# Optimization experiments

Measured on AMD Instinct MI355X. Metric: run time of the kernel, lower is better.

The kernel has to match this reference:

```python
import jax, jax.numpy as jnp
import numpy as np

IN_FEATURE = 4096
OUT_FEATURE = 4096
BLOCK_SIZE = 128
NUM_BLOCKS = IN_FEATURE // BLOCK_SIZE


def setup_inputs() -> dict:
    key = jax.random.key(0)
    k1, k2 = jax.random.split(key)
    x = jax.random.normal(k1, (4, 2048, IN_FEATURE), dtype=jnp.float32)
    # weight laid out as the original nn.Linear: [out_feature, in_feature]
    weight = jax.random.normal(k2, (OUT_FEATURE, IN_FEATURE), dtype=jnp.float32) * (1.0 / np.sqrt(IN_FEATURE))
    return {"x": x, "weight": weight}


def reference(x, weight):
    # The grouped 1x1 conv + reduce-sum over blocks is exactly a blockwise
    # matmul summed over blocks, i.e. out = x @ weight.T.
    # Expressed per-block to mirror the original structure without the
    # conv/permute/reshape overhead:
    b, s, in_f = x.shape
    xb = x.reshape(b, s, NUM_BLOCKS, BLOCK_SIZE)            # [b,s,nb,k]
    wb = weight.reshape(OUT_FEATURE, NUM_BLOCKS, BLOCK_SIZE)  # [o,nb,k]
    # sum over blocks (nb) and block_size (k) == full contraction over in_feature
    out = jnp.einsum('bsnk,onk->bso', xb, wb)
    return out
```

## Files before the change

### kernel.cpp

```cpp
#include <hip/hip_runtime.h>
#include <hip/hip_bf16.h>
#include <stdint.h>


typedef __bf16 bf16x8 __attribute__((ext_vector_type(8)));
typedef float f32x4 __attribute__((ext_vector_type(4)));

__device__ __forceinline__ unsigned short f2bf(float f) {
  unsigned u = __builtin_bit_cast(unsigned, f);
  u += 0x7FFFu + ((u >> 16) & 1u);
  return (unsigned short)(u >> 16);
}

__global__ void cvt_f32_to_bf16(const float* __restrict__ src,
                                unsigned short* __restrict__ dst, long n4) {
  long i = (long)blockIdx.x * blockDim.x + threadIdx.x;
  const long stride = (long)gridDim.x * blockDim.x;
  for (; i < n4; i += stride) {
    float4 v = reinterpret_cast<const float4*>(src)[i];
    ushort4 o;
    o.x = f2bf(v.x); o.y = f2bf(v.y); o.z = f2bf(v.z); o.w = f2bf(v.w);
    reinterpret_cast<ushort4*>(dst)[i] = o;
  }
}

__device__ __forceinline__ void gload_lds16(const void* g, void* lds) {
  __builtin_amdgcn_global_load_lds(
      (__attribute__((address_space(1))) void*)(g),
      (__attribute__((address_space(3))) void*)(lds), 16, 0, 0);
}

#define BARRIER()                                    \
  do {                                               \
    asm volatile("" ::: "memory");                   \
    __builtin_amdgcn_s_barrier();                    \
    asm volatile("" ::: "memory");                   \
  } while (0)
#define WAIT_LGKM0() asm volatile("s_waitcnt lgkmcnt(0)" ::: "memory")
#define WAIT_VM4() asm volatile("s_waitcnt vmcnt(4)" ::: "memory")
#define WAIT_VM0() asm volatile("s_waitcnt vmcnt(0)" ::: "memory")

#define READ_A(AB, LO)                                                      \
  _Pragma("unroll") for (int mi = 0; mi < 4; ++mi) {                        \
    const int row_ = ((LO)*4 + mi) * 16 + lr;                               \
    fa[(LO)*4 + mi][0] = *(const bf16x8*)((AB) + row_ * 128 + sx0);         \
    fa[(LO)*4 + mi][1] = *(const bf16x8*)((AB) + row_ * 128 + sx1);         \
  }
#define READ_B(BB, LO)                                                      \
  _Pragma("unroll") for (int ni = 0; ni < 2; ++ni) {                        \
    const int row_ = brow0 + ((LO)*2 + ni) * 16 + lr;                       \
    fb[(LO)*2 + ni][0] = *(const bf16x8*)((BB) + row_ * 128 + sx0);         \
    fb[(LO)*2 + ni][1] = *(const bf16x8*)((BB) + row_ * 128 + sx1);         \
  }
#define MQ(M0, N0)                                                          \
  _Pragma("unroll") for (int kk = 0; kk < 2; ++kk)                          \
  _Pragma("unroll") for (int mi = 0; mi < 4; ++mi)                          \
  _Pragma("unroll") for (int ni = 0; ni < 2; ++ni)                          \
      acc[(M0) + mi][(N0) + ni] = __builtin_amdgcn_mfma_f32_16x16x32_bf16(  \
          fa[(M0) + mi][kk], fb[(N0) + ni][kk], acc[(M0) + mi][(N0) + ni],  \
          0, 0, 0);

#define PH(READS, STAGES, M0, N0, WAITS)  \
  do {                                    \
    READS STAGES BARRIER();               \
    WAIT_LGKM0();                         \
    __builtin_amdgcn_s_setprio(1);        \
    MQ(M0, N0)                            \
    __builtin_amdgcn_s_setprio(0);        \
    WAITS BARRIER();                      \
  } while (0)

__global__ __launch_bounds__(512, 2) void gemm256(
    const unsigned short* __restrict__ A, const unsigned short* __restrict__ B,
    float* __restrict__ C, int M, int N, int K) {
  __shared__ __attribute__((aligned(1024))) char lds[131072];
  const int A00 = 0, A01 = 16384, A10 = 32768, A11 = 49152;
  const int B00 = 65536, B01 = 81920, B10 = 98304, B11 = 114688;

  const int t = threadIdx.x;
  const int l = t & 63;
  const int w = t >> 6;
  const int wm = w >> 2;
  const int wn = w & 3;
  const int q = l >> 4;
  const int lr = l & 15;
  const int xc = (lr & 7) << 4;
  const int sx0 = (q * 16) ^ xc;
  const int sx1 = (64 + q * 16) ^ xc;
  const int brow0 = (wn & 1) * 64;
  const int srow = l >> 3;
  const int sslot = ((l & 7) ^ ((l >> 3) & 7)) * 8;

  const int nwg = gridDim.x;
  int swz = blockIdx.x;
  if ((nwg & 7) == 0) swz = (swz & 7) * (nwg >> 3) + (swz >> 3);
  const int ntx = N >> 8;
  const int bx = swz % ntx;
  const int by = swz / ntx;
  const int mBase = by * 256, nBase = bx * 256;

  const char* Ard0 = lds + wm * 16384;
  const char* Ard1 = lds + 32768 + wm * 16384;
  const char* Brd0 = lds + 65536 + (wn >> 1) * 16384;
  const char* Brd1 = lds + 98304 + (wn >> 1) * 16384;

  bf16x8 fa[8][2], fb[4][2];
  f32x4 acc[8][4] = {};

  auto STAGE = [&](const unsigned short* __restrict__ G, int row0, int k0,
                   int ldsOff) {
    const unsigned short* s =
        G + (size_t)(row0 + w * 8 + srow) * K + k0 + sslot;
    char* d = lds + ldsOff + w * 1024;
    gload_lds16(s, d);
    gload_lds16(s + (size_t)64 * K, d + 8192);
  };

  STAGE(A, mBase, 0, A00);
  STAGE(A, mBase + 128, 0, A01);
  STAGE(B, nBase, 0, B00);
  STAGE(B, nBase + 128, 0, B01);
  STAGE(B, nBase, 64, B10);
  STAGE(A, mBase, 64, A10);
  WAIT_VM4();
  BARRIER();

  const int itermain = K / 128 - 1;
  for (int i = 0; i < itermain; ++i) {
    const int kA = (2 * i + 1) * 64;
    const int kB = kA + 64;
    const int kC = kB + 64;
    PH(READ_A(Ard0, 0) READ_B(Brd0, 0), STAGE(A, mBase + 128, kA, A11);, 0, 0, );
    PH(READ_B(Brd0, 1),                 STAGE(B, nBase + 128, kA, B11);, 0, 2, );
    PH(READ_A(Ard0, 1),                 STAGE(B, nBase,       kB, B00);, 4, 0, );
    PH(,                                STAGE(A, mBase,       kB, A00);, 4, 2, WAIT_VM4(););
    PH(READ_A(Ard1, 0) READ_B(Brd1, 0), STAGE(A, mBase + 128, kB, A01);, 0, 0, );
    PH(READ_B(Brd1, 1),                 STAGE(B, nBase + 128, kB, B01);, 0, 2, );
    PH(READ_A(Ard1, 1),                 STAGE(B, nBase,       kC, B10);, 4, 0, );
    PH(,                                STAGE(A, mBase,       kC, A10);, 4, 2, WAIT_VM4(););
  }

  {
    const int kT = K - 64;
    PH(READ_A(Ard0, 0) READ_B(Brd0, 0), STAGE(A, mBase + 128, kT, A11);, 0, 0, );
    PH(READ_B(Brd0, 1),                 STAGE(B, nBase + 128, kT, B11);, 0, 2, );
    PH(READ_A(Ard0, 1),                 ,                                4, 0, );
    PH(,                                ,                                4, 2, WAIT_VM0(););
    PH(READ_A(Ard1, 0) READ_B(Brd1, 0), ,                                0, 0, );
    PH(READ_B(Brd1, 1),                 ,                                0, 2, );
    PH(READ_A(Ard1, 1),                 ,                                4, 0, );
    PH(,                                ,                                4, 2, );
  }

  float* Cw = C + (size_t)(mBase + wm * 128 + q * 4) * N + nBase + wn * 64 + lr;
#pragma unroll
  for (int mi = 0; mi < 8; ++mi)
#pragma unroll
    for (int ni = 0; ni < 4; ++ni)
#pragma unroll
      for (int r = 0; r < 4; ++r)
        Cw[(size_t)(mi * 16 + r) * N + ni * 16] = acc[mi][ni][r];
}

typedef unsigned short ushort8f __attribute__((ext_vector_type(8)));
__global__ __launch_bounds__(256) void gemm_fb(
    const float* __restrict__ Af, const float* __restrict__ Wf,
    float* __restrict__ C, int M, int N, int K) {
  __shared__ __attribute__((aligned(16))) unsigned short Ash[128 * 64];
  __shared__ __attribute__((aligned(16))) unsigned short Bsh[128 * 64];
  const int t = threadIdx.x, l = t & 63, w = t >> 6;
  const int mBase = blockIdx.y * 128, nBase = blockIdx.x * 128;
  const int wm = w >> 1, wn = w & 1;
  const int lr = l & 15, lk = (l >> 4) * 8;
  f32x4 acc[4][4] = {};
  const int frow = t >> 1, fkh = (t & 1) * 32;
  for (int k0 = 0; k0 < K; k0 += 64) {
    const float* ga = Af + (size_t)(mBase + frow) * K + k0 + fkh;
    const float* gb = Wf + (size_t)(nBase + frow) * K + k0 + fkh;
#pragma unroll
    for (int j = 0; j < 4; ++j) {
      float4 a0 = reinterpret_cast<const float4*>(ga)[2 * j];
      float4 a1 = reinterpret_cast<const float4*>(ga)[2 * j + 1];
      float4 b0 = reinterpret_cast<const float4*>(gb)[2 * j];
      float4 b1 = reinterpret_cast<const float4*>(gb)[2 * j + 1];
      ushort8f oa = {f2bf(a0.x), f2bf(a0.y), f2bf(a0.z), f2bf(a0.w),
                     f2bf(a1.x), f2bf(a1.y), f2bf(a1.z), f2bf(a1.w)};
      ushort8f ob = {f2bf(b0.x), f2bf(b0.y), f2bf(b0.z), f2bf(b0.w),
                     f2bf(b1.x), f2bf(b1.y), f2bf(b1.z), f2bf(b1.w)};
      *reinterpret_cast<ushort8f*>(&Ash[frow * 64 + fkh + j * 8]) = oa;
      *reinterpret_cast<ushort8f*>(&Bsh[frow * 64 + fkh + j * 8]) = ob;
    }
    __syncthreads();
#pragma unroll
    for (int kk = 0; kk < 2; ++kk) {
      bf16x8 a[4], b[4];
#pragma unroll
      for (int mi = 0; mi < 4; ++mi)
        a[mi] = *reinterpret_cast<const bf16x8*>(
            &Ash[(wm * 64 + mi * 16 + lr) * 64 + kk * 32 + lk]);
#pragma unroll
      for (int ni = 0; ni < 4; ++ni)
        b[ni] = *reinterpret_cast<const bf16x8*>(
            &Bsh[(wn * 64 + ni * 16 + lr) * 64 + kk * 32 + lk]);
#pragma unroll
      for (int mi = 0; mi < 4; ++mi)
#pragma unroll
        for (int ni = 0; ni < 4; ++ni)
          acc[mi][ni] = __builtin_amdgcn_mfma_f32_16x16x32_bf16(
              a[mi], b[ni], acc[mi][ni], 0, 0, 0);
    }
    __syncthreads();
  }
  const int crow0 = mBase + wm * 64 + (l >> 4) * 4;
  const int ccol0 = nBase + wn * 64 + lr;
#pragma unroll
  for (int mi = 0; mi < 4; ++mi)
#pragma unroll
    for (int ni = 0; ni < 4; ++ni)
#pragma unroll
      for (int r = 0; r < 4; ++r)
        C[(size_t)(crow0 + mi * 16 + r) * N + ccol0 + ni * 16] =
            acc[mi][ni][r];
}

extern "C" void kernel_launch(void* const* d_in, const int* in_sizes, int n_in,
                              void* d_out, int out_size, void* d_ws, size_t ws_size,
                              hipStream_t stream) {
  (void)n_in; (void)out_size;
  const float* x = (const float*)d_in[0];
  const float* wgt = (const float*)d_in[1];
  float* out = (float*)d_out;

  const long x_elems = in_sizes[0];
  const long w_elems = in_sizes[1];
  const int K = 4096;
  const int M = (int)(x_elems / K);
  const int N = (int)(w_elems / K);

  const size_t need = (size_t)(x_elems + w_elems) * sizeof(unsigned short);
  const bool ok256 =
      (M % 256 == 0) && (N % 256 == 0) && (K % 128 == 0) && (K >= 256) &&
      ws_size >= need;
  if (ok256) {
    unsigned short* Abf = (unsigned short*)d_ws;
    unsigned short* Wbf = Abf + x_elems;
    cvt_f32_to_bf16<<<2048, 256, 0, stream>>>(x, Abf, x_elems / 4);
    cvt_f32_to_bf16<<<2048, 256, 0, stream>>>(wgt, Wbf, w_elems / 4);
    gemm256<<<dim3((M / 256) * (N / 256)), 512, 0, stream>>>(Abf, Wbf, out, M,
                                                             N, K);
  } else {
    dim3 grid(N / 128, M / 128);
    gemm_fb<<<grid, 256, 0, stream>>>(x, wgt, out, M, N, K);
  }
}
```

Baseline: 274.7 us.

## Switch GEMM inner tiles from 16x16x32 to 32x32x16 bf16 MFMA

Reworks the 256x256 bf16 GEMM so each wave computes with 32x32x16 MFMA instructions instead of 16x16x32. The LDS fragment reads, accumulator layout and output store mapping are rewritten to match, and the explicit lgkmcnt(0) wait before each MFMA group is dropped, leaving the compiler to place the LDS waits. The larger MFMA shape is meant to cut LDS read traffic per FLOP and instruction issue overhead. It risks LDS bank conflicts with the existing XOR swizzle and changes register pressure.

```diff
diff --git a/kernel.cpp b/kernel.cpp
--- a/kernel.cpp
+++ b/kernel.cpp
@@ -5,6 +5,7 @@
 
 typedef __bf16 bf16x8 __attribute__((ext_vector_type(8)));
 typedef float f32x4 __attribute__((ext_vector_type(4)));
+typedef float f32x16 __attribute__((ext_vector_type(16)));
 
 __device__ __forceinline__ unsigned short f2bf(float f) {
   unsigned u = __builtin_bit_cast(unsigned, f);
@@ -36,36 +37,34 @@
     __builtin_amdgcn_s_barrier();                    \
     asm volatile("" ::: "memory");                   \
   } while (0)
-#define WAIT_LGKM0() asm volatile("s_waitcnt lgkmcnt(0)" ::: "memory")
 #define WAIT_VM4() asm volatile("s_waitcnt vmcnt(4)" ::: "memory")
 #define WAIT_VM0() asm volatile("s_waitcnt vmcnt(0)" ::: "memory")
 
-#define READ_A(AB, LO)                                                      \
-  _Pragma("unroll") for (int mi = 0; mi < 4; ++mi) {                        \
-    const int row_ = ((LO)*4 + mi) * 16 + lr;                               \
-    fa[(LO)*4 + mi][0] = *(const bf16x8*)((AB) + row_ * 128 + sx0);         \
-    fa[(LO)*4 + mi][1] = *(const bf16x8*)((AB) + row_ * 128 + sx1);         \
-  }
-#define READ_B(BB, LO)                                                      \
-  _Pragma("unroll") for (int ni = 0; ni < 2; ++ni) {                        \
-    const int row_ = brow0 + ((LO)*2 + ni) * 16 + lr;                       \
-    fb[(LO)*2 + ni][0] = *(const bf16x8*)((BB) + row_ * 128 + sx0);         \
-    fb[(LO)*2 + ni][1] = *(const bf16x8*)((BB) + row_ * 128 + sx1);         \
-  }
-#define MQ(M0, N0)                                                          \
-  _Pragma("unroll") for (int kk = 0; kk < 2; ++kk)                          \
-  _Pragma("unroll") for (int mi = 0; mi < 4; ++mi)                          \
-  _Pragma("unroll") for (int ni = 0; ni < 2; ++ni)                          \
-      acc[(M0) + mi][(N0) + ni] = __builtin_amdgcn_mfma_f32_16x16x32_bf16(  \
-          fa[(M0) + mi][kk], fb[(N0) + ni][kk], acc[(M0) + mi][(N0) + ni],  \
-          0, 0, 0);
-
-#define PH(READS, STAGES, M0, N0, WAITS)  \
+#define READ_A(AB, P)                                                        \
+  _Pragma("unroll") for (int mi = 0; mi < 2; ++mi) {                         \
+    const int row_ = ((P)*2 + mi) * 32 + l31;                                \
+    _Pragma("unroll") for (int ks = 0; ks < 4; ++ks)                         \
+        fa[(P)*2 + mi][ks] =                                                 \
+            *(const bf16x8*)((AB) + row_ * 128 + ((kq + ks * 32) ^ xc));     \
+  }
+#define READ_B(BB, NI)                                                       \
+  {                                                                          \
+    const int row_ = brow0 + (NI)*32 + l31;                                  \
+    _Pragma("unroll") for (int ks = 0; ks < 4; ++ks)                         \
+        fb[NI][ks] =                                                         \
+            *(const bf16x8*)((BB) + row_ * 128 + ((kq + ks * 32) ^ xc));     \
+  }
+#define MQ(P, NI)                                                            \
+  _Pragma("unroll") for (int ks = 0; ks < 4; ++ks)                           \
+  _Pragma("unroll") for (int mi = 0; mi < 2; ++mi)                           \
+      acc[(P)*2 + mi][NI] = __builtin_amdgcn_mfma_f32_32x32x16_bf16(         \
+          fa[(P)*2 + mi][ks], fb[NI][ks], acc[(P)*2 + mi][NI], 0, 0, 0);
+
+#define PH(READS, STAGES, MQCALL, WAITS)  \
   do {                                    \
     READS STAGES BARRIER();               \
-    WAIT_LGKM0();                         \
     __builtin_amdgcn_s_setprio(1);        \
-    MQ(M0, N0)                            \
+    MQCALL                                \
     __builtin_amdgcn_s_setprio(0);        \
     WAITS BARRIER();                      \
   } while (0)
@@ -82,11 +81,9 @@
   const int w = t >> 6;
   const int wm = w >> 2;
   const int wn = w & 3;
-  const int q = l >> 4;
-  const int lr = l & 15;
-  const int xc = (lr & 7) << 4;
-  const int sx0 = (q * 16) ^ xc;
-  const int sx1 = (64 + q * 16) ^ xc;
+  const int l31 = l & 31;
+  const int kq = (l >> 5) * 16;
+  const int xc = (l & 7) << 4;
   const int brow0 = (wn & 1) * 64;
   const int srow = l >> 3;
   const int sslot = ((l & 7) ^ ((l >> 3) & 7)) * 8;
@@ -104,8 +101,8 @@
   const char* Brd0 = lds + 65536 + (wn >> 1) * 16384;
   const char* Brd1 = lds + 98304 + (wn >> 1) * 16384;
 
-  bf16x8 fa[8][2], fb[4][2];
-  f32x4 acc[8][4] = {};
+  bf16x8 fa[4][2 * 2], fb[2][4];
+  f32x16 acc[4][2] = {};
 
   auto STAGE = [&](const unsigned short* __restrict__ G, int row0, int k0,
                    int ldsOff) {
@@ -130,36 +127,38 @@
     const int kA = (2 * i + 1) * 64;
     const int kB = kA + 64;
     const int kC = kB + 64;
-    PH(READ_A(Ard0, 0) READ_B(Brd0, 0), STAGE(A, mBase + 128, kA, A11);, 0, 0, );
-    PH(READ_B(Brd0, 1),                 STAGE(B, nBase + 128, kA, B11);, 0, 2, );
-    PH(READ_A(Ard0, 1),                 STAGE(B, nBase,       kB, B00);, 4, 0, );
-    PH(,                                STAGE(A, mBase,       kB, A00);, 4, 2, WAIT_VM4(););
-    PH(READ_A(Ard1, 0) READ_B(Brd1, 0), STAGE(A, mBase + 128, kB, A01);, 0, 0, );
-    PH(READ_B(Brd1, 1),                 STAGE(B, nBase + 128, kB, B01);, 0, 2, );
-    PH(READ_A(Ard1, 1),                 STAGE(B, nBase,       kC, B10);, 4, 0, );
-    PH(,                                STAGE(A, mBase,       kC, A10);, 4, 2, WAIT_VM4(););
+    PH(READ_A(Ard0, 0) READ_B(Brd0, 0), STAGE(A, mBase + 128, kA, A11);, MQ(0, 0), );
+    PH(READ_B(Brd0, 1),                 STAGE(B, nBase + 128, kA, B11);, MQ(0, 1), );
+    PH(READ_A(Ard0, 1),                 STAGE(B, nBase,       kB, B00);, MQ(1, 0), );
+    PH(,                                STAGE(A, mBase,       kB, A00);, MQ(1, 1), WAIT_VM4(););
+    PH(READ_A(Ard1, 0) READ_B(Brd1, 0), STAGE(A, mBase + 128, kB, A01);, MQ(0, 0), );
+    PH(READ_B(Brd1, 1),                 STAGE(B, nBase + 128, kB, B01);, MQ(0, 1), );
+    PH(READ_A(Ard1, 1),                 STAGE(B, nBase,       kC, B10);, MQ(1, 0), );
+    PH(,                                STAGE(A, mBase,       kC, A10);, MQ(1, 1), WAIT_VM4(););
   }
 
   {
     const int kT = K - 64;
-    PH(READ_A(Ard0, 0) READ_B(Brd0, 0), STAGE(A, mBase + 128, kT, A11);, 0, 0, );
-    PH(READ_B(Brd0, 1),                 STAGE(B, nBase + 128, kT, B11);, 0, 2, );
-    PH(READ_A(Ard0, 1),                 ,                                4, 0, );
-    PH(,                                ,                                4, 2, WAIT_VM0(););
-    PH(READ_A(Ard1, 0) READ_B(Brd1, 0), ,                                0, 0, );
-    PH(READ_B(Brd1, 1),                 ,                                0, 2, );
-    PH(READ_A(Ard1, 1),                 ,                                4, 0, );
-    PH(,                                ,                                4, 2, );
-  }
-
-  float* Cw = C + (size_t)(mBase + wm * 128 + q * 4) * N + nBase + wn * 64 + lr;
-#pragma unroll
-  for (int mi = 0; mi < 8; ++mi)
-#pragma unroll
-    for (int ni = 0; ni < 4; ++ni)
-#pragma unroll
-      for (int r = 0; r < 4; ++r)
-        Cw[(size_t)(mi * 16 + r) * N + ni * 16] = acc[mi][ni][r];
+    PH(READ_A(Ard0, 0) READ_B(Brd0, 0), STAGE(A, mBase + 128, kT, A11);, MQ(0, 0), );
+    PH(READ_B(Brd0, 1),                 STAGE(B, nBase + 128, kT, B11);, MQ(0, 1), );
+    PH(READ_A(Ard0, 1),                 ,                                MQ(1, 0), );
+    PH(,                                ,                                MQ(1, 1), WAIT_VM0(););
+    PH(READ_A(Ard1, 0) READ_B(Brd1, 0), ,                                MQ(0, 0), );
+    PH(READ_B(Brd1, 1),                 ,                                MQ(0, 1), );
+    PH(READ_A(Ard1, 1),                 ,                                MQ(1, 0), );
+    PH(,                                ,                                MQ(1, 1), );
+  }
+
+  const int cl = l & 31, ch = l >> 5;
+  float* Cw = C + (size_t)(mBase + wm * 128 + 4 * ch) * N + nBase + wn * 64 + cl;
+#pragma unroll
+  for (int mi = 0; mi < 4; ++mi)
+#pragma unroll
+    for (int ni = 0; ni < 2; ++ni)
+#pragma unroll
+      for (int r = 0; r < 16; ++r)
+        Cw[(size_t)(mi * 32 + (r & 3) + 8 * (r >> 2)) * N + ni * 32] =
+            acc[mi][ni][r];
 }
 
 typedef unsigned short ushort8f __attribute__((ext_vector_type(8)));
```

Result: slower. 309.2 us (+12.6%).
